# Kernel tuning notes

Measured on AMD Instinct MI355X. Metric: run time of the kernel, lower is better.

## Reference

```python
import jax, jax.numpy as jnp
import numpy as np

B, N, K = 16, 4096, 32

def setup_inputs() -> dict:
    key = jax.random.key(0)
    k0, k1, k2, k3, k4, k5 = jax.random.split(key, 6)
    frames_rot = jax.random.normal(k0, (B, N, 3, 3), jnp.float32)
    frames_trans = jax.random.normal(k1, (B, N, 3), jnp.float32)
    pair_rot = jax.random.normal(k2, (B, N, K, 3, 3), jnp.float32)
    pair_trans = jax.random.normal(k3, (B, N, K, 3), jnp.float32)
    confidences = jax.random.uniform(k4, (B, N, K, 1), jnp.float32)
    topology = jax.random.randint(k5, (B, N, K), 0, N, jnp.int32)
    return {"frames_rot": frames_rot, "frames_trans": frames_trans,
            "pair_rot": pair_rot, "pair_trans": pair_trans,
            "confidences": confidences, "topology": topology}


def _proj_with_svd(m):
    """Kabsch projection of batched [..., 3, 3] matrices onto SO(3) (det=+1)."""
    u, s, vh = jnp.linalg.svd(m, full_matrices=False)
    V = jnp.swapaxes(vh, -1, -2)
    d = jnp.sign(jnp.linalg.det(jnp.matmul(V, jnp.swapaxes(u, -1, -2))))  # [...]
    d3 = jnp.concatenate([jnp.ones(d.shape + (2,), m.dtype), d[..., None]], axis=-1)  # diag(1,1,d)
    # rot = V @ diag(1,1,d) @ u^T
    return jnp.einsum('...ik,...k,...jk->...ij', V, d3, u)


def reference(frames_rot, frames_trans, pair_rot, pair_trans, confidences, topology):
    # gather neighbor frames T_j: [B,N,K,3,3] / [B,N,K,3]
    gather = jax.vmap(lambda f, t: f[t])
    Tj_rot = gather(frames_rot, topology)
    Tj_trans = gather(frames_trans, topology)

    # normalized confidences p_ij over neighbors K
    w = jnp.squeeze(confidences, axis=-1)             # [B,N,K]
    p = w / jnp.sum(w, axis=2, keepdims=True)         # [B,N,K]

    # compose rigids: T_j * T_ji
    comp_rot = jnp.einsum('bnkij,bnkjl->bnkil', Tj_rot, pair_rot)                 # [B,N,K,3,3]
    comp_trans = jnp.einsum('bnkij,bnkj->bnki', Tj_rot, pair_trans) + Tj_trans    # [B,N,K,3]

    # confidence-weighted average over neighbors
    avg_rot = jnp.einsum('bnk,bnkij->bnij', p, comp_rot)    # [B,N,3,3]
    avg_trans = jnp.einsum('bnk,bnki->bni', p, comp_trans)  # [B,N,3]

    # project averaged rot onto SO(3), then invert (transpose) as in the module
    rot = _proj_with_svd(avg_rot)
    rot_inv = jnp.swapaxes(rot, -1, -2)                     # invert_rots of a rotation

    # pack (rot 9 + trans 3) -> [B,N,12]
    return jnp.concatenate([rot_inv.reshape(B, N, 9), avg_trans], axis=-1)
```

## Files before the change

kernel.cpp:

```cpp
#include <hip/hip_runtime.h>
#include <math.h>

#define N_RES 4096
#define KNB 32
#define BN_TOTAL 65536

template <int p, int q>
__device__ __forceinline__ void jacobi_rot(float S[3][3], float V[3][3]) {
    float apq = S[p][q];
    if (fabsf(apq) > 1e-20f) {
        float app = S[p][p], aqq = S[q][q];
        float tau = (aqq - app) / (2.0f * apq);
        float tt = (tau >= 0.0f ? 1.0f : -1.0f) / (fabsf(tau) + sqrtf(1.0f + tau * tau));
        float c = 1.0f / sqrtf(1.0f + tt * tt);
        float s = tt * c;
#pragma unroll
        for (int i = 0; i < 3; i++) {
            float Sip = S[i][p], Siq = S[i][q];
            S[i][p] = c * Sip - s * Siq;
            S[i][q] = s * Sip + c * Siq;
        }
#pragma unroll
        for (int i = 0; i < 3; i++) {
            float Spi = S[p][i], Sqi = S[q][i];
            S[p][i] = c * Spi - s * Sqi;
            S[q][i] = s * Spi + c * Sqi;
        }
#pragma unroll
        for (int i = 0; i < 3; i++) {
            float Vip = V[i][p], Viq = V[i][q];
            V[i][p] = c * Vip - s * Viq;
            V[i][q] = s * Vip + c * Viq;
        }
    }
}

template <int A, int Bc>
__device__ __forceinline__ void sort_pair(float lam[3], float V[3][3]) {
    if (lam[A] < lam[Bc]) {
        float tl = lam[A]; lam[A] = lam[Bc]; lam[Bc] = tl;
#pragma unroll
        for (int i = 0; i < 3; i++) {
            float tv = V[i][A]; V[i][A] = V[i][Bc]; V[i][Bc] = tv;
        }
    }
}

__global__ __launch_bounds__(256) void backbone_kernel(
    const float* __restrict__ frames_rot,
    const float* __restrict__ frames_trans,
    const float* __restrict__ pair_rot,
    const float* __restrict__ pair_trans,
    const float* __restrict__ conf,
    const int* __restrict__ topo,
    float* __restrict__ out)
{
    int g = blockIdx.x * 256 + threadIdx.x;
    int elem = g >> 2;
    int t = g & 3;
    if (elem >= BN_TOTAL) return;
    int b = elem >> 12;

    const float* fr_b = frames_rot + (size_t)b * N_RES * 9;
    const float* ft_b = frames_trans + (size_t)b * N_RES * 3;

    size_t kbase = (size_t)elem * KNB + (size_t)t * 8;
    const float4* pr4 = (const float4*)(pair_rot + kbase * 9);
    const float4* pt4 = (const float4*)(pair_trans + kbase * 3);
    const float4* cf4 = (const float4*)(conf + kbase);
    const int4* tp4 = (const int4*)(topo + kbase);

    float Macc[9] = {0, 0, 0, 0, 0, 0, 0, 0, 0};
    float tacc[3] = {0, 0, 0};
    float wsum = 0.0f;

#pragma unroll
    for (int c = 0; c < 2; c++) {
        float prl[36];
#pragma unroll
        for (int i = 0; i < 9; i++) {
            float4 v = pr4[c * 9 + i];
            prl[4 * i + 0] = v.x; prl[4 * i + 1] = v.y;
            prl[4 * i + 2] = v.z; prl[4 * i + 3] = v.w;
        }
        float ptl[12];
#pragma unroll
        for (int i = 0; i < 3; i++) {
            float4 v = pt4[c * 3 + i];
            ptl[4 * i + 0] = v.x; ptl[4 * i + 1] = v.y;
            ptl[4 * i + 2] = v.z; ptl[4 * i + 3] = v.w;
        }
        float4 wv = cf4[c];
        float wl[4] = {wv.x, wv.y, wv.z, wv.w};
        int4 jv = tp4[c];
        int jl[4] = {jv.x, jv.y, jv.z, jv.w};

#pragma unroll
        for (int kk = 0; kk < 4; kk++) {
            int j = jl[kk];
            const float* Rj = fr_b + j * 9;
            const float* Tj = ft_b + j * 3;
            float r[9];
#pragma unroll
            for (int i = 0; i < 9; i++) r[i] = Rj[i];
            float tj[3];
#pragma unroll
            for (int i = 0; i < 3; i++) tj[i] = Tj[i];
            float w = wl[kk];
            const float* pr = prl + kk * 9;
            const float* pt = ptl + kk * 3;
#pragma unroll
            for (int i = 0; i < 3; i++) {
#pragma unroll
                for (int l = 0; l < 3; l++) {
                    float cij = r[i * 3 + 0] * pr[0 * 3 + l] +
                                r[i * 3 + 1] * pr[1 * 3 + l] +
                                r[i * 3 + 2] * pr[2 * 3 + l];
                    Macc[i * 3 + l] += w * cij;
                }
                float ct = r[i * 3 + 0] * pt[0] + r[i * 3 + 1] * pt[1] +
                           r[i * 3 + 2] * pt[2] + tj[i];
                tacc[i] += w * ct;
            }
            wsum += w;
        }
    }

#pragma unroll
    for (int i = 0; i < 9; i++) Macc[i] += __shfl_xor(Macc[i], 1);
#pragma unroll
    for (int i = 0; i < 3; i++) tacc[i] += __shfl_xor(tacc[i], 1);
    wsum += __shfl_xor(wsum, 1);
#pragma unroll
    for (int i = 0; i < 9; i++) Macc[i] += __shfl_xor(Macc[i], 2);
#pragma unroll
    for (int i = 0; i < 3; i++) tacc[i] += __shfl_xor(tacc[i], 2);
    wsum += __shfl_xor(wsum, 2);

    float inv_w = 1.0f / fmaxf(wsum, 1e-20f);
    float M[3][3];
#pragma unroll
    for (int i = 0; i < 3; i++)
#pragma unroll
        for (int j = 0; j < 3; j++) M[i][j] = Macc[i * 3 + j] * inv_w;
    float t0 = tacc[0] * inv_w, t1 = tacc[1] * inv_w, t2 = tacc[2] * inv_w;

    float S[3][3];
#pragma unroll
    for (int i = 0; i < 3; i++)
#pragma unroll
        for (int j = 0; j < 3; j++)
            S[i][j] = M[0][i] * M[0][j] + M[1][i] * M[1][j] + M[2][i] * M[2][j];
    float V[3][3] = {{1, 0, 0}, {0, 1, 0}, {0, 0, 1}};

#pragma unroll
    for (int sweep = 0; sweep < 4; sweep++) {
        jacobi_rot<0, 1>(S, V);
        jacobi_rot<0, 2>(S, V);
        jacobi_rot<1, 2>(S, V);
    }

    float lam[3] = {S[0][0], S[1][1], S[2][2]};
    sort_pair<0, 1>(lam, V);
    sort_pair<1, 2>(lam, V);
    sort_pair<0, 1>(lam, V);

    float detV = V[0][0] * (V[1][1] * V[2][2] - V[1][2] * V[2][1]) -
                 V[0][1] * (V[1][0] * V[2][2] - V[1][2] * V[2][0]) +
                 V[0][2] * (V[1][0] * V[2][1] - V[1][1] * V[2][0]);
    if (detV < 0.0f) { V[0][2] = -V[0][2]; V[1][2] = -V[1][2]; V[2][2] = -V[2][2]; }

    float Bm[3][3];
#pragma unroll
    for (int i = 0; i < 3; i++)
#pragma unroll
        for (int j = 0; j < 3; j++)
            Bm[i][j] = M[i][0] * V[0][j] + M[i][1] * V[1][j] + M[i][2] * V[2][j];

    float u0[3] = {Bm[0][0], Bm[1][0], Bm[2][0]};
    float n0 = u0[0] * u0[0] + u0[1] * u0[1] + u0[2] * u0[2];
    float rn0 = 1.0f / sqrtf(fmaxf(n0, 1e-24f));
    u0[0] *= rn0; u0[1] *= rn0; u0[2] *= rn0;

    float b1[3] = {Bm[0][1], Bm[1][1], Bm[2][1]};
    float d01 = u0[0] * b1[0] + u0[1] * b1[1] + u0[2] * b1[2];
    float u1[3] = {b1[0] - d01 * u0[0], b1[1] - d01 * u0[1], b1[2] - d01 * u0[2]};
    float n1 = u1[0] * u1[0] + u1[1] * u1[1] + u1[2] * u1[2];
    float rn1 = 1.0f / sqrtf(fmaxf(n1, 1e-24f));
    u1[0] *= rn1; u1[1] *= rn1; u1[2] *= rn1;

    float u2[3] = {u0[1] * u1[2] - u0[2] * u1[1],
                   u0[2] * u1[0] - u0[0] * u1[2],
                   u0[0] * u1[1] - u0[1] * u1[0]};

    float R[9];
#pragma unroll
    for (int i = 0; i < 3; i++) {
        float Ui0 = (i == 0 ? u0[0] : (i == 1 ? u0[1] : u0[2]));
        float Ui1 = (i == 0 ? u1[0] : (i == 1 ? u1[1] : u1[2]));
        float Ui2 = (i == 0 ? u2[0] : (i == 1 ? u2[1] : u2[2]));
#pragma unroll
        for (int j = 0; j < 3; j++)
            R[i * 3 + j] = Ui0 * V[j][0] + Ui1 * V[j][1] + Ui2 * V[j][2];
    }

    if (t == 0) {
        float4* o4 = (float4*)(out + (size_t)elem * 12);
        o4[0] = make_float4(R[0], R[1], R[2], R[3]);
        o4[1] = make_float4(R[4], R[5], R[6], R[7]);
        o4[2] = make_float4(R[8], t0, t1, t2);
    }
}

extern "C" void kernel_launch(void* const* d_in, const int* in_sizes, int n_in,
                              void* d_out, int out_size, void* d_ws, size_t ws_size,
                              hipStream_t stream) {
    const float* frames_rot = (const float*)d_in[0];
    const float* frames_trans = (const float*)d_in[1];
    const float* pair_rot = (const float*)d_in[2];
    const float* pair_trans = (const float*)d_in[3];
    const float* conf = (const float*)d_in[4];
    const int* topo = (const int*)d_in[5];
    float* out = (float*)d_out;

    dim3 grid(BN_TOTAL * 4 / 256), block(256);
    hipLaunchKernelGGL(backbone_kernel, grid, block, 0, stream,
                       frames_rot, frames_trans, pair_rot, pair_trans, conf, topo, out);
}
```

Measured before the change: 197.5 us.

## Use 8 threads per residue with XCD-aware batch mapping and nontemporal loads

Each residue is now split across 8 threads of 4 neighbors each instead of 4 threads of 8, which doubles the grid and adds a third shuffle-reduction stage. Block IDs are remapped so that all blocks of one batch land on the same XCD (bid & 7), keeping that batch's frames_rot and frames_trans gather table resident in one L2. The streaming pair_rot, pair_trans, confidence and topology loads use nontemporal hints so they do not evict the gathered frames. The cost is more threads doing the redundant SVD and more shuffle work per residue.

```diff
diff --git a/kernel.cpp b/kernel.cpp
--- a/kernel.cpp
+++ b/kernel.cpp
@@ -4,6 +4,9 @@
 #define N_RES 4096
 #define KNB 32
 #define BN_TOTAL 65536
+
+typedef float v4f __attribute__((ext_vector_type(4)));
+typedef int v4i __attribute__((ext_vector_type(4)));
 
 template <int p, int q>
 __device__ __forceinline__ void jacobi_rot(float S[3][3], float V[3][3]) {
@@ -55,87 +58,87 @@
     const int* __restrict__ topo,
     float* __restrict__ out)
 {
-    int g = blockIdx.x * 256 + threadIdx.x;
-    int elem = g >> 2;
-    int t = g & 3;
-    if (elem >= BN_TOTAL) return;
-    int b = elem >> 12;
-
-    const float* fr_b = frames_rot + (size_t)b * N_RES * 9;
-    const float* ft_b = frames_trans + (size_t)b * N_RES * 3;
-
-    size_t kbase = (size_t)elem * KNB + (size_t)t * 8;
-    const float4* pr4 = (const float4*)(pair_rot + kbase * 9);
-    const float4* pt4 = (const float4*)(pair_trans + kbase * 3);
-    const float4* cf4 = (const float4*)(conf + kbase);
-    const int4* tp4 = (const int4*)(topo + kbase);
+    int tid = threadIdx.x;
+    int bid = blockIdx.x;
+
+    int xcd = bid & 7;
+    int slot = bid >> 3;
+    int batch = xcd + ((slot >> 7) << 3);
+    int chunk = slot & 127;
+
+    int elem = batch * N_RES + chunk * 32 + (tid >> 3);
+    int t = tid & 7;
+
+    const float* fr_b = frames_rot + (size_t)batch * N_RES * 9;
+    const float* ft_b = frames_trans + (size_t)batch * N_RES * 3;
+
+    size_t kbase = (size_t)elem * KNB + (size_t)t * 4;
+    const v4f* pr4 = (const v4f*)(pair_rot + kbase * 9);
+    const v4f* pt4 = (const v4f*)(pair_trans + kbase * 3);
+    const v4f* cf4 = (const v4f*)(conf + kbase);
+    const v4i* tp4 = (const v4i*)(topo + kbase);
+
+    float prl[36];
+#pragma unroll
+    for (int i = 0; i < 9; i++) {
+        v4f v = __builtin_nontemporal_load(pr4 + i);
+        prl[4 * i + 0] = v.x; prl[4 * i + 1] = v.y;
+        prl[4 * i + 2] = v.z; prl[4 * i + 3] = v.w;
+    }
+    float ptl[12];
+#pragma unroll
+    for (int i = 0; i < 3; i++) {
+        v4f v = __builtin_nontemporal_load(pt4 + i);
+        ptl[4 * i + 0] = v.x; ptl[4 * i + 1] = v.y;
+        ptl[4 * i + 2] = v.z; ptl[4 * i + 3] = v.w;
+    }
+    v4f wv = __builtin_nontemporal_load(cf4);
+    float wl[4] = {wv.x, wv.y, wv.z, wv.w};
+    v4i jv = __builtin_nontemporal_load(tp4);
+    int jl[4] = {jv.x, jv.y, jv.z, jv.w};
 
     float Macc[9] = {0, 0, 0, 0, 0, 0, 0, 0, 0};
     float tacc[3] = {0, 0, 0};
     float wsum = 0.0f;
 
 #pragma unroll
-    for (int c = 0; c < 2; c++) {
-        float prl[36];
-#pragma unroll
-        for (int i = 0; i < 9; i++) {
-            float4 v = pr4[c * 9 + i];
-            prl[4 * i + 0] = v.x; prl[4 * i + 1] = v.y;
-            prl[4 * i + 2] = v.z; prl[4 * i + 3] = v.w;
-        }
-        float ptl[12];
-#pragma unroll
-        for (int i = 0; i < 3; i++) {
-            float4 v = pt4[c * 3 + i];
-            ptl[4 * i + 0] = v.x; ptl[4 * i + 1] = v.y;
-            ptl[4 * i + 2] = v.z; ptl[4 * i + 3] = v.w;
-        }
-        float4 wv = cf4[c];
-        float wl[4] = {wv.x, wv.y, wv.z, wv.w};
-        int4 jv = tp4[c];
-        int jl[4] = {jv.x, jv.y, jv.z, jv.w};
-
-#pragma unroll
-        for (int kk = 0; kk < 4; kk++) {
-            int j = jl[kk];
-            const float* Rj = fr_b + j * 9;
-            const float* Tj = ft_b + j * 3;
-            float r[9];
-#pragma unroll
-            for (int i = 0; i < 9; i++) r[i] = Rj[i];
-            float tj[3];
-#pragma unroll
-            for (int i = 0; i < 3; i++) tj[i] = Tj[i];
-            float w = wl[kk];
-            const float* pr = prl + kk * 9;
-            const float* pt = ptl + kk * 3;
-#pragma unroll
-            for (int i = 0; i < 3; i++) {
-#pragma unroll
-                for (int l = 0; l < 3; l++) {
-                    float cij = r[i * 3 + 0] * pr[0 * 3 + l] +
-                                r[i * 3 + 1] * pr[1 * 3 + l] +
-                                r[i * 3 + 2] * pr[2 * 3 + l];
-                    Macc[i * 3 + l] += w * cij;
-                }
-                float ct = r[i * 3 + 0] * pt[0] + r[i * 3 + 1] * pt[1] +
-                           r[i * 3 + 2] * pt[2] + tj[i];
-                tacc[i] += w * ct;
+    for (int kk = 0; kk < 4; kk++) {
+        int j = jl[kk];
+        const float* Rj = fr_b + j * 9;
+        const float* Tj = ft_b + j * 3;
+        float r[9];
+#pragma unroll
+        for (int i = 0; i < 9; i++) r[i] = Rj[i];
+        float tj[3];
+#pragma unroll
+        for (int i = 0; i < 3; i++) tj[i] = Tj[i];
+        float w = wl[kk];
+        const float* pr = prl + kk * 9;
+        const float* pt = ptl + kk * 3;
+#pragma unroll
+        for (int i = 0; i < 3; i++) {
+#pragma unroll
+            for (int l = 0; l < 3; l++) {
+                float cij = r[i * 3 + 0] * pr[0 * 3 + l] +
+                            r[i * 3 + 1] * pr[1 * 3 + l] +
+                            r[i * 3 + 2] * pr[2 * 3 + l];
+                Macc[i * 3 + l] += w * cij;
             }
-            wsum += w;
-        }
-    }
-
-#pragma unroll
-    for (int i = 0; i < 9; i++) Macc[i] += __shfl_xor(Macc[i], 1);
-#pragma unroll
-    for (int i = 0; i < 3; i++) tacc[i] += __shfl_xor(tacc[i], 1);
-    wsum += __shfl_xor(wsum, 1);
-#pragma unroll
-    for (int i = 0; i < 9; i++) Macc[i] += __shfl_xor(Macc[i], 2);
-#pragma unroll
-    for (int i = 0; i < 3; i++) tacc[i] += __shfl_xor(tacc[i], 2);
-    wsum += __shfl_xor(wsum, 2);
+            float ct = r[i * 3 + 0] * pt[0] + r[i * 3 + 1] * pt[1] +
+                       r[i * 3 + 2] * pt[2] + tj[i];
+            tacc[i] += w * ct;
+        }
+        wsum += w;
+    }
+
+#pragma unroll
+    for (int st = 1; st <= 4; st <<= 1) {
+#pragma unroll
+        for (int i = 0; i < 9; i++) Macc[i] += __shfl_xor(Macc[i], st);
+#pragma unroll
+        for (int i = 0; i < 3; i++) tacc[i] += __shfl_xor(tacc[i], st);
+        wsum += __shfl_xor(wsum, st);
+    }
 
     float inv_w = 1.0f / fmaxf(wsum, 1e-20f);
     float M[3][3];
@@ -223,7 +226,7 @@
     const int* topo = (const int*)d_in[5];
     float* out = (float*)d_out;
 
-    dim3 grid(BN_TOTAL * 4 / 256), block(256);
+    dim3 grid(BN_TOTAL * 8 / 256), block(256);
     hipLaunchKernelGGL(backbone_kernel, grid, block, 0, stream,
                        frames_rot, frames_trans, pair_rot, pair_trans, conf, topo, out);
 }
```

After: 198.2 us. No clear change (+0.3%).
